# Kernel optimization log

Hardware: AMD Instinct MI355X
Metric: run time of the kernel (lower is better)

## Reference

```python
import jax, jax.numpy as jnp
import numpy as np

NMS_THR = 0.3


def pairwise_iou(b):
    # b: [N,4] in x1,y1,x2,y2
    area = (b[:, 2] - b[:, 0]) * (b[:, 3] - b[:, 1])  # [N]
    x1 = jnp.maximum(b[:, None, 0], b[None, :, 0])
    y1 = jnp.maximum(b[:, None, 1], b[None, :, 1])
    x2 = jnp.minimum(b[:, None, 2], b[None, :, 2])
    y2 = jnp.minimum(b[:, None, 3], b[None, :, 3])
    inter = jnp.clip(x2 - x1, 0.0) * jnp.clip(y2 - y1, 0.0)
    return inter / (area[:, None] + area[None, :] - inter + 1e-9)


def nms_keep(boxes, scores, valid, thr):
    # greedy NMS, fixed-shape: returns bool keep mask in original order
    N = boxes.shape[0]
    order = jnp.argsort(-jnp.where(valid, scores, -jnp.inf))
    b = boxes[order]
    v = valid[order]
    iou = pairwise_iou(b)  # [N,N]

    def step(keep, i):
        suppressed = jnp.any(keep & (iou[i] > thr))
        keep = keep.at[i].set(v[i] & jnp.logical_not(suppressed))
        return keep, None

    keep_sorted, _ = jax.lax.scan(step, jnp.zeros((N,), dtype=bool), jnp.arange(N))
    return jnp.zeros((N,), dtype=bool).at[order].set(keep_sorted)


def setup_inputs() -> dict:
    key = jax.random.key(0)
    k1, k2, k3, k4 = jax.random.split(key, 4)
    N, C, S = 6000, 81, 800
    # well-formed proposals: x1,y1 in [0, 600), w,h in [8, 200)
    xy = jax.random.uniform(k1, (N, 2), dtype=jnp.float32) * 600.0
    wh = 8.0 + jax.random.uniform(k2, (N, 2), dtype=jnp.float32) * 192.0
    proposals = jnp.concatenate([xy, xy + wh], axis=1)  # [N,4]
    reg = jax.random.normal(k3, (N, C * 4), dtype=jnp.float32)
    clss = jax.random.normal(k4, (N, C), dtype=jnp.float32) * 2.0
    stds = jnp.array([0.1, 0.1, 0.2, 0.2], dtype=jnp.float32)
    return {"proposals": proposals, "reg": reg, "clss": clss, "stds": stds, "img_size": S}


def reference(proposals, reg, clss, stds, img_size):
    N, C = clss.shape
    # anchors_bbox2offset: x1y1x2y2 -> center x,y + w,h
    w = proposals[:, 2] - proposals[:, 0]
    h = proposals[:, 3] - proposals[:, 1]
    cx = proposals[:, 0] + 0.5 * w
    cy = proposals[:, 1] + 0.5 * h
    # class selection
    probs = jax.nn.softmax(clss, axis=1)
    cls_idx = jnp.argmax(probs, axis=1)  # [N]
    score = jnp.take_along_axis(probs, cls_idx[:, None], axis=1)[:, 0]
    valid = cls_idx != 0  # non-background
    reg4 = reg.reshape(N, C, 4)
    t = jnp.take_along_axis(reg4, cls_idx[:, None, None], axis=1)[:, 0, :] * stds  # [N,4]
    # decode
    px = cx + w * t[:, 0]
    py = cy + h * t[:, 1]
    pw = w * jnp.exp(t[:, 2])
    ph = h * jnp.exp(t[:, 3])
    # offset2bbox + clip
    hi = jnp.float32(img_size - 1)
    x1 = jnp.clip(px - 0.5 * pw, 0.0, hi)
    y1 = jnp.clip(py - 0.5 * ph, 0.0, hi)
    x2 = jnp.clip(px + 0.5 * pw, 0.0, hi)
    y2 = jnp.clip(py + 0.5 * ph, 0.0, hi)
    boxes = jnp.stack((x1, y1, x2, y2), axis=1)  # [N,4]
    keep = nms_keep(jax.lax.stop_gradient(boxes), jax.lax.stop_gradient(score), valid, NMS_THR)
    m = keep.astype(boxes.dtype)
    return boxes * m[:, None], score * m, cls_idx * keep.astype(cls_idx.dtype)
```

## Files before the change

### kernel.cpp

```cpp
#include <hip/hip_runtime.h>
#include <math.h>

#define NMS_THR 0.3f
#define NACC 8

__device__ __forceinline__ float fmul(float a, float b){ return __fmul_rn(a,b); }
__device__ __forceinline__ float fadd(float a, float b){ return __fadd_rn(a,b); }
__device__ __forceinline__ float fsub(float a, float b){ return __fsub_rn(a,b); }

#define BAR_LDS() asm volatile("s_waitcnt lgkmcnt(0)\n\ts_barrier" ::: "memory")

__device__ __forceinline__ unsigned long long rfl64(unsigned long long x){
    unsigned int lo = (unsigned int)__builtin_amdgcn_readfirstlane((int)(unsigned int)x);
    unsigned int hi = (unsigned int)__builtin_amdgcn_readfirstlane((int)(unsigned int)(x >> 32));
    return ((unsigned long long)hi << 32) | lo;
}

__global__ __launch_bounds__(256) void k_decode(
    const float* __restrict__ prop, const float* __restrict__ reg,
    const float* __restrict__ clss, const float* __restrict__ stds,
    const int* __restrict__ imgsz,
    float* __restrict__ boxes, float* __restrict__ key,
    float* __restrict__ score, int* __restrict__ cls,
    int N, int C)
{
    int wid  = threadIdx.x >> 6;
    int lane = threadIdx.x & 63;
    int n = blockIdx.x * 4 + wid;
    if (n >= N) return;
    const float* row = clss + (long)n * C;
    float ninf = -__builtin_inff();
    float x0 = (lane < C)      ? row[lane]      : ninf;
    float x1 = (lane + 64 < C) ? row[lane + 64] : ninf;
    float m = fmaxf(x0, x1);
    for (int o = 32; o > 0; o >>= 1) m = fmaxf(m, __shfl_xor(m, o));
    float e0 = (lane < C)      ? expf(x0 - m) : 0.0f;
    float e1 = (lane + 64 < C) ? expf(x1 - m) : 0.0f;
    float s = e0 + e1;
    for (int o = 32; o > 0; o >>= 1) s += __shfl_xor(s, o);
    float bv; int bi;
    if (e0 >= e1) { bv = e0; bi = lane; } else { bv = e1; bi = lane + 64; }
    for (int o = 32; o > 0; o >>= 1) {
        float ov = __shfl_xor(bv, o);
        int   oi = __shfl_xor(bi, o);
        if (ov > bv || (ov == bv && oi < bi)) { bv = ov; bi = oi; }
    }
    if (lane == 0) {
        float sc = 1.0f / s;
        int   c  = bi;
        int   valid = (c != 0);
        float p0 = prop[n*4+0], p1 = prop[n*4+1], p2 = prop[n*4+2], p3 = prop[n*4+3];
        float w  = fsub(p2, p0), h = fsub(p3, p1);
        float cx = fadd(p0, fmul(0.5f, w));
        float cy = fadd(p1, fmul(0.5f, h));
        const float* rr = reg + (long)n * C * 4 + (long)c * 4;
        float t0 = fmul(rr[0], stds[0]);
        float t1 = fmul(rr[1], stds[1]);
        float t2 = fmul(rr[2], stds[2]);
        float t3 = fmul(rr[3], stds[3]);
        float px = fadd(cx, fmul(w, t0));
        float py = fadd(cy, fmul(h, t1));
        float pw = fmul(w, expf(t2));
        float ph = fmul(h, expf(t3));
        float hi = (float)(imgsz[0] - 1);
        float bx1 = fminf(fmaxf(fsub(px, fmul(0.5f, pw)), 0.0f), hi);
        float by1 = fminf(fmaxf(fsub(py, fmul(0.5f, ph)), 0.0f), hi);
        float bx2 = fminf(fmaxf(fadd(px, fmul(0.5f, pw)), 0.0f), hi);
        float by2 = fminf(fmaxf(fadd(py, fmul(0.5f, ph)), 0.0f), hi);
        boxes[n*4+0]=bx1; boxes[n*4+1]=by1; boxes[n*4+2]=bx2; boxes[n*4+3]=by2;
        score[n] = sc;
        cls[n]   = c;
        key[n]   = valid ? sc : ninf;
    }
}

__global__ __launch_bounds__(256) void k_rank(
    const float* __restrict__ key, const float* __restrict__ boxes,
    float* __restrict__ boxesSorted, float* __restrict__ areaSorted,
    float* __restrict__ keySorted, int* __restrict__ rank,
    int* __restrict__ nValidPtr, int N)
{
    extern __shared__ float lkey[];
    __shared__ int part[256];
    int tid = threadIdx.x;
    for (int j = tid; j < N; j += 256) lkey[j] = key[j];
    __syncthreads();

    int i = blockIdx.x * 64 + (tid & 63);
    int s = tid >> 6;
    int Q = (N + 3) >> 2;
    int r_part = 0;
    if (i < N) {
        float ki = lkey[i];
        int j0 = s * Q, j1 = min(N, j0 + Q);
        for (int j = j0; j < j1; ++j) {
            float kj = lkey[j];
            r_part += (kj > ki) || (kj == ki && j < i);
        }
    }
    part[tid] = r_part;
    __syncthreads();

    if (tid < 64 && i < N) {
        int r = part[tid] + part[tid+64] + part[tid+128] + part[tid+192];
        float ki = lkey[i];
        rank[i] = r;
        float b0 = boxes[i*4+0], b1 = boxes[i*4+1], b2 = boxes[i*4+2], b3 = boxes[i*4+3];
        boxesSorted[r*4+0]=b0; boxesSorted[r*4+1]=b1; boxesSorted[r*4+2]=b2; boxesSorted[r*4+3]=b3;
        areaSorted[r] = fmul(fsub(b2,b0), fsub(b3,b1));
        keySorted[r]  = ki;
    }

    if (blockIdx.x == 0) {
        __syncthreads();
        float ninf = -__builtin_inff();
        int inv = 0;
        for (int j = tid; j < N; j += 256) inv += (lkey[j] == ninf);
        part[tid] = inv;
        __syncthreads();
        if (tid == 0) {
            int t = 0;
            for (int q = 0; q < 256; ++q) t += part[q];
            nValidPtr[0] = N - t;
        }
    }
}

__global__ __launch_bounds__(256) void k_mask(
    const float* __restrict__ bs, const float* __restrict__ areas,
    const float* __restrict__ keySorted, unsigned long long* __restrict__ mask,
    unsigned long long* __restrict__ bq,
    int N, int W, int Wpad)
{
    int wid  = threadIdx.x >> 6;
    int lane = threadIdx.x & 63;
    int i = blockIdx.x * 4 + wid;
    if (i >= N) return;
    if (keySorted[i] == -__builtin_inff()) return;
    float ax1 = bs[i*4+0], ay1 = bs[i*4+1], ax2 = bs[i*4+2], ay2 = bs[i*4+3];
    float aa  = areas[i];
    int w0 = i >> 6;
#pragma unroll
    for (int k = 1; k <= 3; ++k) {
        unsigned long long bm = 0ULL;
        if (w0 - k >= 0) {
            int j = (w0 - k) * 64 + lane;
            float bx1 = bs[j*4+0], by1 = bs[j*4+1], bx2 = bs[j*4+2], by2 = bs[j*4+3];
            float ba  = areas[j];
            float ix1 = fmaxf(ax1,bx1), iy1 = fmaxf(ay1,by1);
            float ix2 = fminf(ax2,bx2), iy2 = fminf(ay2,by2);
            float iw = fmaxf(fsub(ix2,ix1), 0.0f);
            float ih = fmaxf(fsub(iy2,iy1), 0.0f);
            float inter = fmul(iw, ih);
            float denom = fadd(fsub(fadd(aa, ba), inter), 1e-9f);
            float iou = inter / denom;
            bm = __ballot(iou > NMS_THR);
        }
        if (lane == 0) bq[(size_t)i*4 + k] = bm;
    }
    for (int w = w0; w < W; ++w) {
        int j = w*64 + lane;
        int bit = 0;
        if (j < N && j != i) {
            float bx1 = bs[j*4+0], by1 = bs[j*4+1], bx2 = bs[j*4+2], by2 = bs[j*4+3];
            float ba  = areas[j];
            float ix1 = fmaxf(ax1,bx1), iy1 = fmaxf(ay1,by1);
            float ix2 = fminf(ax2,bx2), iy2 = fminf(ay2,by2);
            float iw = fmaxf(fsub(ix2,ix1), 0.0f);
            float ih = fmaxf(fsub(iy2,iy1), 0.0f);
            float inter = fmul(iw, ih);
            float denom = fadd(fsub(fadd(aa, ba), inter), 1e-9f);
            float iou = inter / denom;
            bit = (iou > NMS_THR) ? 1 : 0;
        }
        unsigned long long fwd = __ballot(bit && (j > i));
        if (w == w0) {
            unsigned long long bwd = __ballot(bit && (j < i));
            if (lane == 0) {
                mask[(long)i*Wpad + w] = fwd;
                bq[(size_t)i*4 + 0] = bwd;
            }
        } else {
            if (lane == 0) mask[(long)i*Wpad + w] = fwd;
        }
    }
}

__global__ __launch_bounds__((NACC+1)*64, 1) void k_scan(
    const unsigned long long* __restrict__ mask,
    const unsigned long long* __restrict__ bq,
    const int* __restrict__ nValidPtr,
    int* __restrict__ keepSorted, int N, int W, int Wpad)
{
    __shared__ unsigned long long ldsPartA[NACC+1];
    __shared__ unsigned long long ldsPartB[NACC+1];
    __shared__ unsigned long long ldsKeepLo, ldsKeepHi;
    int tid  = threadIdx.x;
    int wid  = tid >> 6;
    int lane = tid & 63;
    for (int i = tid; i < N; i += (NACC+1)*64) keepSorted[i] = 0;
    if (tid <= NACC) { ldsPartA[tid] = 0ULL; ldsPartB[tid] = 0ULL; }
    if (tid == 0) { ldsKeepLo = 0ULL; ldsKeepHi = 0ULL; }
    __syncthreads();

    int nValid  = __builtin_amdgcn_readfirstlane(nValidPtr[0]);
    int nChunks = (nValid + 127) >> 7;

    unsigned long long a0=0,a1=0,a2=0,a3=0, b0=0,b1=0,b2=0,b3=0;
    unsigned long long keepLoPrev = 0ULL, keepHiPrev = 0ULL;
    if (wid == 0 && nChunks > 0) {
        int rA = lane, rB = 64 + lane;
        if (rA < N) {
            ulonglong2 q01 = *(const ulonglong2*)(bq + (size_t)rA*4);
            ulonglong2 q23 = *(const ulonglong2*)(bq + (size_t)rA*4 + 2);
            a0=q01.x; a1=q01.y; a2=q23.x; a3=q23.y;
        }
        if (rB < N) {
            ulonglong2 q01 = *(const ulonglong2*)(bq + (size_t)rB*4);
            ulonglong2 q23 = *(const ulonglong2*)(bq + (size_t)rB*4 + 2);
            b0=q01.x; b1=q01.y; b2=q23.x; b3=q23.y;
        }
    }
    unsigned long long accx = 0ULL, accy = 0ULL;
    bool accWave = (wid >= 1);
    int  accIdx  = wid - 1;
    bool laneok  = (2*lane + 1 < Wpad);

    for (int c = 0; c < nChunks; ++c) {
        int base = c << 7;
        if (wid == 0) {
            unsigned long long na0=0,na1=0,na2=0,na3=0, nb0=0,nb1=0,nb2=0,nb3=0;
            if (c + 1 < nChunks) {
                int rA = base + 128 + lane, rB = base + 192 + lane;
                if (rA < N) {
                    ulonglong2 q01 = *(const ulonglong2*)(bq + (size_t)rA*4);
                    ulonglong2 q23 = *(const ulonglong2*)(bq + (size_t)rA*4 + 2);
                    na0=q01.x; na1=q01.y; na2=q23.x; na3=q23.y;
                }
                if (rB < N) {
                    ulonglong2 q01 = *(const ulonglong2*)(bq + (size_t)rB*4);
                    ulonglong2 q23 = *(const ulonglong2*)(bq + (size_t)rB*4 + 2);
                    nb0=q01.x; nb1=q01.y; nb2=q23.x; nb3=q23.y;
                }
            }

            unsigned long long pA = 0ULL, pB = 0ULL;
#pragma unroll
            for (int k = 1; k <= NACC; ++k) { pA |= ldsPartA[k]; pB |= ldsPartB[k]; }
            unsigned long long prevLo =
                __ballot(((a1 & keepHiPrev) | (a2 & keepLoPrev)) != 0ULL);
            unsigned long long prevHi =
                __ballot(((b2 & keepHiPrev) | (b3 & keepLoPrev)) != 0ULL);
            unsigned long long incLo = rfl64(pA) | prevLo;
            unsigned long long incHi = rfl64(pB) | prevHi;
            int nv  = nValid - base;
            unsigned long long validLo = (nv >= 64) ? ~0ULL : ((1ULL << nv) - 1ULL);
            int nv2 = nv - 64;
            unsigned long long validHi = (nv2 >= 64) ? ~0ULL
                                        : (nv2 <= 0 ? 0ULL : ((1ULL << nv2) - 1ULL));
            unsigned long long candLo = validLo & ~incLo;
            unsigned long long candHi = validHi & ~incHi;
            unsigned long long keepLo = 0ULL, keepHi = 0ULL;

            while (candLo) {
                int f = __builtin_ctzll(candLo);
                unsigned long long sup = __ballot(((a0 >> f) & 1ULL) != 0ULL);
                unsigned long long b = 1ULL << f;
                keepLo |= b;
                candLo &= ~sup & ~b;
            }
            candHi &= ~__ballot((b1 & keepLo) != 0ULL);
            while (candHi) {
                int f = __builtin_ctzll(candHi);
                unsigned long long sup = __ballot(((b0 >> f) & 1ULL) != 0ULL);
                unsigned long long b = 1ULL << f;
                keepHi |= b;
                candHi &= ~sup & ~b;
            }
            keepLoPrev = keepLo; keepHiPrev = keepHi;
            if (lane == 0) { ldsKeepLo = keepLo; ldsKeepHi = keepHi; }
            if (base + lane < N)      keepSorted[base + lane]      = (int)((keepLo >> lane) & 1ULL);
            if (base + 64 + lane < N) keepSorted[base + 64 + lane] = (int)((keepHi >> lane) & 1ULL);
            a0=na0; a1=na1; a2=na2; a3=na3; b0=nb0; b1=nb1; b2=nb2; b3=nb3;
        }
        BAR_LDS();
        unsigned long long kLo = ldsKeepLo;
        unsigned long long kHi = ldsKeepHi;
        if (accWave && laneok && lane == c + 1) {
            ldsPartA[wid] = accx;
            ldsPartB[wid] = accy;
        }
        BAR_LDS();
        if (accWave && laneok) {
            unsigned int myb = (accIdx < 4)
                ? (unsigned int)((kLo >> (16*accIdx)) & 0xFFFFULL)
                : (unsigned int)((kHi >> (16*(accIdx-4))) & 0xFFFFULL);
            if (myb) {
                const unsigned long long* mb =
                    mask + (size_t)(base + 16*accIdx) * Wpad + 2*lane;
                unsigned int b = myb;
                int q0 = __builtin_ctz(b); b &= b - 1;
                int q1=-1,q2=-1,q3=-1,q4=-1,q5=-1,q6=-1,q7=-1;
                if (b) { q1 = __builtin_ctz(b); b &= b - 1; }
                if (b) { q2 = __builtin_ctz(b); b &= b - 1; }
                if (b) { q3 = __builtin_ctz(b); b &= b - 1; }
                if (b) { q4 = __builtin_ctz(b); b &= b - 1; }
                if (b) { q5 = __builtin_ctz(b); b &= b - 1; }
                if (b) { q6 = __builtin_ctz(b); b &= b - 1; }
                if (b) { q7 = __builtin_ctz(b); b &= b - 1; }
                ulonglong2 v0 = {0,0}, v1 = {0,0}, v2 = {0,0}, v3 = {0,0};
                ulonglong2 v4 = {0,0}, v5 = {0,0}, v6 = {0,0}, v7 = {0,0};
                v0 = *(const ulonglong2*)(mb + (size_t)q0 * Wpad);
                if (q1 >= 0) v1 = *(const ulonglong2*)(mb + (size_t)q1 * Wpad);
                if (q2 >= 0) v2 = *(const ulonglong2*)(mb + (size_t)q2 * Wpad);
                if (q3 >= 0) v3 = *(const ulonglong2*)(mb + (size_t)q3 * Wpad);
                if (q4 >= 0) v4 = *(const ulonglong2*)(mb + (size_t)q4 * Wpad);
                if (q5 >= 0) v5 = *(const ulonglong2*)(mb + (size_t)q5 * Wpad);
                if (q6 >= 0) v6 = *(const ulonglong2*)(mb + (size_t)q6 * Wpad);
                if (q7 >= 0) v7 = *(const ulonglong2*)(mb + (size_t)q7 * Wpad);
                accx |= ((v0.x|v1.x)|(v2.x|v3.x)) | ((v4.x|v5.x)|(v6.x|v7.x));
                accy |= ((v0.y|v1.y)|(v2.y|v3.y)) | ((v4.y|v5.y)|(v6.y|v7.y));
                while (b) {
                    int a = __builtin_ctz(b); b &= b - 1;
                    ulonglong2 v = *(const ulonglong2*)(mb + (size_t)a * Wpad);
                    accx |= v.x; accy |= v.y;
                }
            }
        }
    }
}

__global__ __launch_bounds__(256) void k_out(
    const float* __restrict__ boxes, const float* __restrict__ score,
    const int* __restrict__ cls, const int* __restrict__ rank,
    const int* __restrict__ keepSorted,
    float* __restrict__ out, int N)
{
    int n = blockIdx.x * blockDim.x + threadIdx.x;
    if (n >= N) return;
    int k = keepSorted[rank[n]];
    float m = (float)k;
    out[n*4+0] = boxes[n*4+0]*m;
    out[n*4+1] = boxes[n*4+1]*m;
    out[n*4+2] = boxes[n*4+2]*m;
    out[n*4+3] = boxes[n*4+3]*m;
    out[(long)N*4 + n] = score[n]*m;
    out[(long)N*5 + n] = (float)(cls[n] * k);
}

extern "C" void kernel_launch(void* const* d_in, const int* in_sizes, int n_in,
                              void* d_out, int out_size, void* d_ws, size_t ws_size,
                              hipStream_t stream) {
    const float* prop = (const float*)d_in[0];
    const float* reg  = (const float*)d_in[1];
    const float* clss = (const float*)d_in[2];
    const float* stds = (const float*)d_in[3];
    const int*   img  = (const int*)d_in[4];

    int N = in_sizes[0] / 4;
    int C = in_sizes[2] / N;
    int W = (N + 63) / 64;
    int Wpad = (W + 1) & ~1;

    char* ws = (char*)d_ws;
    size_t off = 0;
    float* boxes       = (float*)(ws + off); off += (size_t)N*4*sizeof(float);
    float* key         = (float*)(ws + off); off += (size_t)N*sizeof(float);
    float* score       = (float*)(ws + off); off += (size_t)N*sizeof(float);
    int*   cls         = (int*)  (ws + off); off += (size_t)N*sizeof(int);
    int*   rank        = (int*)  (ws + off); off += (size_t)N*sizeof(int);
    float* boxesSorted = (float*)(ws + off); off += (size_t)N*4*sizeof(float);
    float* areaSorted  = (float*)(ws + off); off += (size_t)N*sizeof(float);
    float* keySorted   = (float*)(ws + off); off += (size_t)N*sizeof(float);
    int*   keepSorted  = (int*)  (ws + off); off += (size_t)N*sizeof(int);
    int*   nValid      = (int*)  (ws + off); off += sizeof(int);
    off = (off + 31) & ~(size_t)31;
    unsigned long long* bq    = (unsigned long long*)(ws + off);
    off += (size_t)N * 4 * sizeof(unsigned long long);
    unsigned long long* mask  = (unsigned long long*)(ws + off);
    off += (size_t)N * Wpad * sizeof(unsigned long long);
    (void)ws_size; (void)out_size; (void)n_in;

    int rowBlocks  = (N + 3) / 4;
    int thrBlocks  = (N + 255) / 256;
    int rankBlocks = (N + 63) / 64;

    k_decode<<<rowBlocks, 256, 0, stream>>>(prop, reg, clss, stds, img,
                                            boxes, key, score, cls, N, C);
    k_rank<<<rankBlocks, 256, (size_t)N*sizeof(float), stream>>>(key, boxes,
                                            boxesSorted, areaSorted, keySorted, rank, nValid, N);
    k_mask<<<rowBlocks, 256, 0, stream>>>(boxesSorted, areaSorted, keySorted,
                                          mask, bq, N, W, Wpad);
    k_scan<<<1, (NACC+1)*64, 0, stream>>>(mask, bq, nValid, keepSorted, N, W, Wpad);
    k_out<<<thrBlocks, 256, 0, stream>>>(boxes, score, cls, rank, keepSorted,
                                         (float*)d_out, N);
}
```

Measured before the change: 170.7 us.

## Fuse five NMS kernels into one cooperative persistent kernel with grid syncs

```diff
diff --git a/kernel.cpp b/kernel.cpp
--- a/kernel.cpp
+++ b/kernel.cpp
@@ -1,8 +1,13 @@
 #include <hip/hip_runtime.h>
+#include <hip/hip_cooperative_groups.h>
 #include <math.h>
+
+namespace cg = cooperative_groups;
 
 #define NMS_THR 0.3f
 #define NACC 8
+#define NBLK 256
+#define NTHR 576
 
 __device__ __forceinline__ float fmul(float a, float b){ return __fmul_rn(a,b); }
 __device__ __forceinline__ float fadd(float a, float b){ return __fadd_rn(a,b); }
@@ -16,347 +21,338 @@
     return ((unsigned long long)hi << 32) | lo;
 }
 
-__global__ __launch_bounds__(256) void k_decode(
-    const float* __restrict__ prop, const float* __restrict__ reg,
-    const float* __restrict__ clss, const float* __restrict__ stds,
-    const int* __restrict__ imgsz,
-    float* __restrict__ boxes, float* __restrict__ key,
-    float* __restrict__ score, int* __restrict__ cls,
-    int N, int C)
+struct Params {
+    const float *prop, *reg, *clss, *stds;
+    const int *img;
+    float *boxes, *key, *score;
+    int *cls, *rank;
+    float *boxesSorted, *areaSorted, *keySorted;
+    int *keepSorted, *nValid;
+    unsigned long long *bq, *mask;
+    float *out;
+    int N, C, W, Wpad, rankBlocks;
+};
+
+__global__ __launch_bounds__(NTHR, 1) void k_all(Params p)
 {
-    int wid  = threadIdx.x >> 6;
-    int lane = threadIdx.x & 63;
-    int n = blockIdx.x * 4 + wid;
-    if (n >= N) return;
-    const float* row = clss + (long)n * C;
-    float ninf = -__builtin_inff();
-    float x0 = (lane < C)      ? row[lane]      : ninf;
-    float x1 = (lane + 64 < C) ? row[lane + 64] : ninf;
-    float m = fmaxf(x0, x1);
-    for (int o = 32; o > 0; o >>= 1) m = fmaxf(m, __shfl_xor(m, o));
-    float e0 = (lane < C)      ? expf(x0 - m) : 0.0f;
-    float e1 = (lane + 64 < C) ? expf(x1 - m) : 0.0f;
-    float s = e0 + e1;
-    for (int o = 32; o > 0; o >>= 1) s += __shfl_xor(s, o);
-    float bv; int bi;
-    if (e0 >= e1) { bv = e0; bi = lane; } else { bv = e1; bi = lane + 64; }
-    for (int o = 32; o > 0; o >>= 1) {
-        float ov = __shfl_xor(bv, o);
-        int   oi = __shfl_xor(bi, o);
-        if (ov > bv || (ov == bv && oi < bi)) { bv = ov; bi = oi; }
-    }
-    if (lane == 0) {
-        float sc = 1.0f / s;
-        int   c  = bi;
-        int   valid = (c != 0);
-        float p0 = prop[n*4+0], p1 = prop[n*4+1], p2 = prop[n*4+2], p3 = prop[n*4+3];
-        float w  = fsub(p2, p0), h = fsub(p3, p1);
-        float cx = fadd(p0, fmul(0.5f, w));
-        float cy = fadd(p1, fmul(0.5f, h));
-        const float* rr = reg + (long)n * C * 4 + (long)c * 4;
-        float t0 = fmul(rr[0], stds[0]);
-        float t1 = fmul(rr[1], stds[1]);
-        float t2 = fmul(rr[2], stds[2]);
-        float t3 = fmul(rr[3], stds[3]);
-        float px = fadd(cx, fmul(w, t0));
-        float py = fadd(cy, fmul(h, t1));
-        float pw = fmul(w, expf(t2));
-        float ph = fmul(h, expf(t3));
-        float hi = (float)(imgsz[0] - 1);
-        float bx1 = fminf(fmaxf(fsub(px, fmul(0.5f, pw)), 0.0f), hi);
-        float by1 = fminf(fmaxf(fsub(py, fmul(0.5f, ph)), 0.0f), hi);
-        float bx2 = fminf(fmaxf(fadd(px, fmul(0.5f, pw)), 0.0f), hi);
-        float by2 = fminf(fmaxf(fadd(py, fmul(0.5f, ph)), 0.0f), hi);
-        boxes[n*4+0]=bx1; boxes[n*4+1]=by1; boxes[n*4+2]=bx2; boxes[n*4+3]=by2;
-        score[n] = sc;
-        cls[n]   = c;
-        key[n]   = valid ? sc : ninf;
-    }
-}
-
-__global__ __launch_bounds__(256) void k_rank(
-    const float* __restrict__ key, const float* __restrict__ boxes,
-    float* __restrict__ boxesSorted, float* __restrict__ areaSorted,
-    float* __restrict__ keySorted, int* __restrict__ rank,
-    int* __restrict__ nValidPtr, int N)
-{
-    extern __shared__ float lkey[];
-    __shared__ int part[256];
-    int tid = threadIdx.x;
-    for (int j = tid; j < N; j += 256) lkey[j] = key[j];
-    __syncthreads();
-
-    int i = blockIdx.x * 64 + (tid & 63);
-    int s = tid >> 6;
-    int Q = (N + 3) >> 2;
-    int r_part = 0;
-    if (i < N) {
-        float ki = lkey[i];
-        int j0 = s * Q, j1 = min(N, j0 + Q);
-        for (int j = j0; j < j1; ++j) {
-            float kj = lkey[j];
-            r_part += (kj > ki) || (kj == ki && j < i);
-        }
-    }
-    part[tid] = r_part;
-    __syncthreads();
-
-    if (tid < 64 && i < N) {
-        int r = part[tid] + part[tid+64] + part[tid+128] + part[tid+192];
-        float ki = lkey[i];
-        rank[i] = r;
-        float b0 = boxes[i*4+0], b1 = boxes[i*4+1], b2 = boxes[i*4+2], b3 = boxes[i*4+3];
-        boxesSorted[r*4+0]=b0; boxesSorted[r*4+1]=b1; boxesSorted[r*4+2]=b2; boxesSorted[r*4+3]=b3;
-        areaSorted[r] = fmul(fsub(b2,b0), fsub(b3,b1));
-        keySorted[r]  = ki;
-    }
-
-    if (blockIdx.x == 0) {
+    cg::grid_group grid = cg::this_grid();
+    extern __shared__ char smem[];
+    const int tid  = threadIdx.x;
+    const int bid  = blockIdx.x;
+    const int wi   = tid >> 6;
+    const int lane = tid & 63;
+    const int gwave  = bid * (NTHR/64) + wi;
+    const int nWaves = gridDim.x * (NTHR/64);
+    const int N = p.N, C = p.C, W = p.W, Wpad = p.Wpad;
+    const float ninf = -__builtin_inff();
+
+    for (int n = gwave; n < N; n += nWaves) {
+        const float* row = p.clss + (long)n * C;
+        float x0 = (lane < C)      ? row[lane]      : ninf;
+        float x1 = (lane + 64 < C) ? row[lane + 64] : ninf;
+        float m = fmaxf(x0, x1);
+        for (int o = 32; o > 0; o >>= 1) m = fmaxf(m, __shfl_xor(m, o));
+        float e0 = (lane < C)      ? expf(x0 - m) : 0.0f;
+        float e1 = (lane + 64 < C) ? expf(x1 - m) : 0.0f;
+        float s = e0 + e1;
+        for (int o = 32; o > 0; o >>= 1) s += __shfl_xor(s, o);
+        float bv; int bi;
+        if (e0 >= e1) { bv = e0; bi = lane; } else { bv = e1; bi = lane + 64; }
+        for (int o = 32; o > 0; o >>= 1) {
+            float ov = __shfl_xor(bv, o);
+            int   oi = __shfl_xor(bi, o);
+            if (ov > bv || (ov == bv && oi < bi)) { bv = ov; bi = oi; }
+        }
+        if (lane == 0) {
+            float sc = 1.0f / s;
+            int   c  = bi;
+            int   valid = (c != 0);
+            float p0 = p.prop[n*4+0], p1 = p.prop[n*4+1];
+            float p2 = p.prop[n*4+2], p3 = p.prop[n*4+3];
+            float w  = fsub(p2, p0), h = fsub(p3, p1);
+            float cx = fadd(p0, fmul(0.5f, w));
+            float cy = fadd(p1, fmul(0.5f, h));
+            const float* rr = p.reg + (long)n * C * 4 + (long)c * 4;
+            float t0 = fmul(rr[0], p.stds[0]);
+            float t1 = fmul(rr[1], p.stds[1]);
+            float t2 = fmul(rr[2], p.stds[2]);
+            float t3 = fmul(rr[3], p.stds[3]);
+            float px = fadd(cx, fmul(w, t0));
+            float py = fadd(cy, fmul(h, t1));
+            float pw = fmul(w, expf(t2));
+            float ph = fmul(h, expf(t3));
+            float hi = (float)(p.img[0] - 1);
+            float bx1 = fminf(fmaxf(fsub(px, fmul(0.5f, pw)), 0.0f), hi);
+            float by1 = fminf(fmaxf(fsub(py, fmul(0.5f, ph)), 0.0f), hi);
+            float bx2 = fminf(fmaxf(fadd(px, fmul(0.5f, pw)), 0.0f), hi);
+            float by2 = fminf(fmaxf(fadd(py, fmul(0.5f, ph)), 0.0f), hi);
+            p.boxes[n*4+0]=bx1; p.boxes[n*4+1]=by1;
+            p.boxes[n*4+2]=bx2; p.boxes[n*4+3]=by2;
+            p.score[n] = sc;
+            p.cls[n]   = c;
+            p.key[n]   = valid ? sc : ninf;
+        }
+    }
+    grid.sync();
+
+    {
+        float* lkey = (float*)smem;
+        int*   part = (int*)(smem + (size_t)N*sizeof(float));
+        if (bid < p.rankBlocks) {
+            for (int j = tid; j < N; j += NTHR) lkey[j] = p.key[j];
+            __syncthreads();
+            int i = bid * 64 + lane;
+            int Q = (N + 8) / 9;
+            int r_part = 0;
+            if (i < N) {
+                float ki = lkey[i];
+                int j0 = wi * Q, j1 = min(N, j0 + Q);
+                for (int j = j0; j < j1; ++j) {
+                    float kj = lkey[j];
+                    r_part += (kj > ki) || (kj == ki && j < i);
+                }
+            }
+            part[tid] = r_part;
+            __syncthreads();
+            if (tid < 64 && i < N) {
+                int r = 0;
+#pragma unroll
+                for (int sIdx = 0; sIdx < 9; ++sIdx) r += part[tid + 64*sIdx];
+                float ki = lkey[i];
+                p.rank[i] = r;
+                float b0 = p.boxes[i*4+0], b1 = p.boxes[i*4+1];
+                float b2 = p.boxes[i*4+2], b3 = p.boxes[i*4+3];
+                p.boxesSorted[r*4+0]=b0; p.boxesSorted[r*4+1]=b1;
+                p.boxesSorted[r*4+2]=b2; p.boxesSorted[r*4+3]=b3;
+                p.areaSorted[r] = fmul(fsub(b2,b0), fsub(b3,b1));
+                p.keySorted[r]  = ki;
+            }
+            if (bid == 0) {
+                __syncthreads();
+                int inv = 0;
+                for (int j = tid; j < N; j += NTHR) inv += (lkey[j] == ninf);
+                part[tid] = inv;
+                __syncthreads();
+                if (tid == 0) {
+                    int t = 0;
+                    for (int q = 0; q < NTHR; ++q) t += part[q];
+                    p.nValid[0] = N - t;
+                }
+            }
+        }
+    }
+    grid.sync();
+
+    for (int i = gwave; i < N; i += nWaves) {
+        if (p.keySorted[i] == ninf) continue;
+        const float* bs = p.boxesSorted;
+        float ax1 = bs[i*4+0], ay1 = bs[i*4+1], ax2 = bs[i*4+2], ay2 = bs[i*4+3];
+        float aa  = p.areaSorted[i];
+        int w0 = i >> 6;
+#pragma unroll
+        for (int k = 1; k <= 3; ++k) {
+            unsigned long long bm = 0ULL;
+            if (w0 - k >= 0) {
+                int j = (w0 - k) * 64 + lane;
+                float bx1 = bs[j*4+0], by1 = bs[j*4+1], bx2 = bs[j*4+2], by2 = bs[j*4+3];
+                float ba  = p.areaSorted[j];
+                float ix1 = fmaxf(ax1,bx1), iy1 = fmaxf(ay1,by1);
+                float ix2 = fminf(ax2,bx2), iy2 = fminf(ay2,by2);
+                float iw = fmaxf(fsub(ix2,ix1), 0.0f);
+                float ih = fmaxf(fsub(iy2,iy1), 0.0f);
+                float inter = fmul(iw, ih);
+                float denom = fadd(fsub(fadd(aa, ba), inter), 1e-9f);
+                float iou = inter / denom;
+                bm = __ballot(iou > NMS_THR);
+            }
+            if (lane == 0) p.bq[(size_t)i*4 + k] = bm;
+        }
+        for (int w = w0; w < W; ++w) {
+            int j = w*64 + lane;
+            int bit = 0;
+            if (j < N && j != i) {
+                float bx1 = bs[j*4+0], by1 = bs[j*4+1], bx2 = bs[j*4+2], by2 = bs[j*4+3];
+                float ba  = p.areaSorted[j];
+                float ix1 = fmaxf(ax1,bx1), iy1 = fmaxf(ay1,by1);
+                float ix2 = fminf(ax2,bx2), iy2 = fminf(ay2,by2);
+                float iw = fmaxf(fsub(ix2,ix1), 0.0f);
+                float ih = fmaxf(fsub(iy2,iy1), 0.0f);
+                float inter = fmul(iw, ih);
+                float denom = fadd(fsub(fadd(aa, ba), inter), 1e-9f);
+                float iou = inter / denom;
+                bit = (iou > NMS_THR) ? 1 : 0;
+            }
+            unsigned long long fwd = __ballot(bit && (j > i));
+            if (w == w0) {
+                unsigned long long bwd = __ballot(bit && (j < i));
+                if (lane == 0) {
+                    p.mask[(long)i*Wpad + w] = fwd;
+                    p.bq[(size_t)i*4 + 0] = bwd;
+                }
+            } else {
+                if (lane == 0) p.mask[(long)i*Wpad + w] = fwd;
+            }
+        }
+    }
+    grid.sync();
+
+    if (bid == 0) {
+        __shared__ unsigned long long ldsPartA[NACC+1];
+        __shared__ unsigned long long ldsPartB[NACC+1];
+        __shared__ unsigned long long ldsKeepLo, ldsKeepHi;
+        const unsigned long long* mask = p.mask;
+        const unsigned long long* bq   = p.bq;
+        int* keepSorted = p.keepSorted;
+        for (int i = tid; i < N; i += NTHR) keepSorted[i] = 0;
+        if (tid <= NACC) { ldsPartA[tid] = 0ULL; ldsPartB[tid] = 0ULL; }
+        if (tid == 0) { ldsKeepLo = 0ULL; ldsKeepHi = 0ULL; }
         __syncthreads();
-        float ninf = -__builtin_inff();
-        int inv = 0;
-        for (int j = tid; j < N; j += 256) inv += (lkey[j] == ninf);
-        part[tid] = inv;
-        __syncthreads();
-        if (tid == 0) {
-            int t = 0;
-            for (int q = 0; q < 256; ++q) t += part[q];
-            nValidPtr[0] = N - t;
-        }
-    }
-}
-
-__global__ __launch_bounds__(256) void k_mask(
-    const float* __restrict__ bs, const float* __restrict__ areas,
-    const float* __restrict__ keySorted, unsigned long long* __restrict__ mask,
-    unsigned long long* __restrict__ bq,
-    int N, int W, int Wpad)
-{
-    int wid  = threadIdx.x >> 6;
-    int lane = threadIdx.x & 63;
-    int i = blockIdx.x * 4 + wid;
-    if (i >= N) return;
-    if (keySorted[i] == -__builtin_inff()) return;
-    float ax1 = bs[i*4+0], ay1 = bs[i*4+1], ax2 = bs[i*4+2], ay2 = bs[i*4+3];
-    float aa  = areas[i];
-    int w0 = i >> 6;
+
+        int nValid  = __builtin_amdgcn_readfirstlane(p.nValid[0]);
+        int nChunks = (nValid + 127) >> 7;
+
+        unsigned long long a0=0,a1=0,a2=0,a3=0, b0=0,b1=0,b2=0,b3=0;
+        unsigned long long keepLoPrev = 0ULL, keepHiPrev = 0ULL;
+        if (wi == 0 && nChunks > 0) {
+            int rA = lane, rB = 64 + lane;
+            if (rA < N) {
+                ulonglong2 q01 = *(const ulonglong2*)(bq + (size_t)rA*4);
+                ulonglong2 q23 = *(const ulonglong2*)(bq + (size_t)rA*4 + 2);
+                a0=q01.x; a1=q01.y; a2=q23.x; a3=q23.y;
+            }
+            if (rB < N) {
+                ulonglong2 q01 = *(const ulonglong2*)(bq + (size_t)rB*4);
+                ulonglong2 q23 = *(const ulonglong2*)(bq + (size_t)rB*4 + 2);
+                b0=q01.x; b1=q01.y; b2=q23.x; b3=q23.y;
+            }
+        }
+        unsigned long long accx = 0ULL, accy = 0ULL;
+        bool accWave = (wi >= 1);
+        int  accIdx  = wi - 1;
+        bool laneok  = (2*lane + 1 < Wpad);
+
+        for (int c = 0; c < nChunks; ++c) {
+            int base = c << 7;
+            if (wi == 0) {
+                unsigned long long na0=0,na1=0,na2=0,na3=0, nb0=0,nb1=0,nb2=0,nb3=0;
+                if (c + 1 < nChunks) {
+                    int rA = base + 128 + lane, rB = base + 192 + lane;
+                    if (rA < N) {
+                        ulonglong2 q01 = *(const ulonglong2*)(bq + (size_t)rA*4);
+                        ulonglong2 q23 = *(const ulonglong2*)(bq + (size_t)rA*4 + 2);
+                        na0=q01.x; na1=q01.y; na2=q23.x; na3=q23.y;
+                    }
+                    if (rB < N) {
+                        ulonglong2 q01 = *(const ulonglong2*)(bq + (size_t)rB*4);
+                        ulonglong2 q23 = *(const ulonglong2*)(bq + (size_t)rB*4 + 2);
+                        nb0=q01.x; nb1=q01.y; nb2=q23.x; nb3=q23.y;
+                    }
+                }
+
+                unsigned long long pA = 0ULL, pB = 0ULL;
 #pragma unroll
-    for (int k = 1; k <= 3; ++k) {
-        unsigned long long bm = 0ULL;
-        if (w0 - k >= 0) {
-            int j = (w0 - k) * 64 + lane;
-            float bx1 = bs[j*4+0], by1 = bs[j*4+1], bx2 = bs[j*4+2], by2 = bs[j*4+3];
-            float ba  = areas[j];
-            float ix1 = fmaxf(ax1,bx1), iy1 = fmaxf(ay1,by1);
-            float ix2 = fminf(ax2,bx2), iy2 = fminf(ay2,by2);
-            float iw = fmaxf(fsub(ix2,ix1), 0.0f);
-            float ih = fmaxf(fsub(iy2,iy1), 0.0f);
-            float inter = fmul(iw, ih);
-            float denom = fadd(fsub(fadd(aa, ba), inter), 1e-9f);
-            float iou = inter / denom;
-            bm = __ballot(iou > NMS_THR);
-        }
-        if (lane == 0) bq[(size_t)i*4 + k] = bm;
-    }
-    for (int w = w0; w < W; ++w) {
-        int j = w*64 + lane;
-        int bit = 0;
-        if (j < N && j != i) {
-            float bx1 = bs[j*4+0], by1 = bs[j*4+1], bx2 = bs[j*4+2], by2 = bs[j*4+3];
-            float ba  = areas[j];
-            float ix1 = fmaxf(ax1,bx1), iy1 = fmaxf(ay1,by1);
-            float ix2 = fminf(ax2,bx2), iy2 = fminf(ay2,by2);
-            float iw = fmaxf(fsub(ix2,ix1), 0.0f);
-            float ih = fmaxf(fsub(iy2,iy1), 0.0f);
-            float inter = fmul(iw, ih);
-            float denom = fadd(fsub(fadd(aa, ba), inter), 1e-9f);
-            float iou = inter / denom;
-            bit = (iou > NMS_THR) ? 1 : 0;
-        }
-        unsigned long long fwd = __ballot(bit && (j > i));
-        if (w == w0) {
-            unsigned long long bwd = __ballot(bit && (j < i));
-            if (lane == 0) {
-                mask[(long)i*Wpad + w] = fwd;
-                bq[(size_t)i*4 + 0] = bwd;
-            }
-        } else {
-            if (lane == 0) mask[(long)i*Wpad + w] = fwd;
-        }
-    }
-}
-
-__global__ __launch_bounds__((NACC+1)*64, 1) void k_scan(
-    const unsigned long long* __restrict__ mask,
-    const unsigned long long* __restrict__ bq,
-    const int* __restrict__ nValidPtr,
-    int* __restrict__ keepSorted, int N, int W, int Wpad)
-{
-    __shared__ unsigned long long ldsPartA[NACC+1];
-    __shared__ unsigned long long ldsPartB[NACC+1];
-    __shared__ unsigned long long ldsKeepLo, ldsKeepHi;
-    int tid  = threadIdx.x;
-    int wid  = tid >> 6;
-    int lane = tid & 63;
-    for (int i = tid; i < N; i += (NACC+1)*64) keepSorted[i] = 0;
-    if (tid <= NACC) { ldsPartA[tid] = 0ULL; ldsPartB[tid] = 0ULL; }
-    if (tid == 0) { ldsKeepLo = 0ULL; ldsKeepHi = 0ULL; }
-    __syncthreads();
-
-    int nValid  = __builtin_amdgcn_readfirstlane(nValidPtr[0]);
-    int nChunks = (nValid + 127) >> 7;
-
-    unsigned long long a0=0,a1=0,a2=0,a3=0, b0=0,b1=0,b2=0,b3=0;
-    unsigned long long keepLoPrev = 0ULL, keepHiPrev = 0ULL;
-    if (wid == 0 && nChunks > 0) {
-        int rA = lane, rB = 64 + lane;
-        if (rA < N) {
-            ulonglong2 q01 = *(const ulonglong2*)(bq + (size_t)rA*4);
-            ulonglong2 q23 = *(const ulonglong2*)(bq + (size_t)rA*4 + 2);
-            a0=q01.x; a1=q01.y; a2=q23.x; a3=q23.y;
-        }
-        if (rB < N) {
-            ulonglong2 q01 = *(const ulonglong2*)(bq + (size_t)rB*4);
-            ulonglong2 q23 = *(const ulonglong2*)(bq + (size_t)rB*4 + 2);
-            b0=q01.x; b1=q01.y; b2=q23.x; b3=q23.y;
-        }
-    }
-    unsigned long long accx = 0ULL, accy = 0ULL;
-    bool accWave = (wid >= 1);
-    int  accIdx  = wid - 1;
-    bool laneok  = (2*lane + 1 < Wpad);
-
-    for (int c = 0; c < nChunks; ++c) {
-        int base = c << 7;
-        if (wid == 0) {
-            unsigned long long na0=0,na1=0,na2=0,na3=0, nb0=0,nb1=0,nb2=0,nb3=0;
-            if (c + 1 < nChunks) {
-                int rA = base + 128 + lane, rB = base + 192 + lane;
-                if (rA < N) {
-                    ulonglong2 q01 = *(const ulonglong2*)(bq + (size_t)rA*4);
-                    ulonglong2 q23 = *(const ulonglong2*)(bq + (size_t)rA*4 + 2);
-                    na0=q01.x; na1=q01.y; na2=q23.x; na3=q23.y;
-                }
-                if (rB < N) {
-                    ulonglong2 q01 = *(const ulonglong2*)(bq + (size_t)rB*4);
-                    ulonglong2 q23 = *(const ulonglong2*)(bq + (size_t)rB*4 + 2);
-                    nb0=q01.x; nb1=q01.y; nb2=q23.x; nb3=q23.y;
-                }
-            }
-
-            unsigned long long pA = 0ULL, pB = 0ULL;
-#pragma unroll
-            for (int k = 1; k <= NACC; ++k) { pA |= ldsPartA[k]; pB |= ldsPartB[k]; }
-            unsigned long long prevLo =
-                __ballot(((a1 & keepHiPrev) | (a2 & keepLoPrev)) != 0ULL);
-            unsigned long long prevHi =
-                __ballot(((b2 & keepHiPrev) | (b3 & keepLoPrev)) != 0ULL);
-            unsigned long long incLo = rfl64(pA) | prevLo;
-            unsigned long long incHi = rfl64(pB) | prevHi;
-            int nv  = nValid - base;
-            unsigned long long validLo = (nv >= 64) ? ~0ULL : ((1ULL << nv) - 1ULL);
-            int nv2 = nv - 64;
-            unsigned long long validHi = (nv2 >= 64) ? ~0ULL
-                                        : (nv2 <= 0 ? 0ULL : ((1ULL << nv2) - 1ULL));
-            unsigned long long candLo = validLo & ~incLo;
-            unsigned long long candHi = validHi & ~incHi;
-            unsigned long long keepLo = 0ULL, keepHi = 0ULL;
-
-            while (candLo) {
-                int f = __builtin_ctzll(candLo);
-                unsigned long long sup = __ballot(((a0 >> f) & 1ULL) != 0ULL);
-                unsigned long long b = 1ULL << f;
-                keepLo |= b;
-                candLo &= ~sup & ~b;
-            }
-            candHi &= ~__ballot((b1 & keepLo) != 0ULL);
-            while (candHi) {
-                int f = __builtin_ctzll(candHi);
-                unsigned long long sup = __ballot(((b0 >> f) & 1ULL) != 0ULL);
-                unsigned long long b = 1ULL << f;
-                keepHi |= b;
-                candHi &= ~sup & ~b;
-            }
-            keepLoPrev = keepLo; keepHiPrev = keepHi;
-            if (lane == 0) { ldsKeepLo = keepLo; ldsKeepHi = keepHi; }
-            if (base + lane < N)      keepSorted[base + lane]      = (int)((keepLo >> lane) & 1ULL);
-            if (base + 64 + lane < N) keepSorted[base + 64 + lane] = (int)((keepHi >> lane) & 1ULL);
-            a0=na0; a1=na1; a2=na2; a3=na3; b0=nb0; b1=nb1; b2=nb2; b3=nb3;
-        }
-        BAR_LDS();
-        unsigned long long kLo = ldsKeepLo;
-        unsigned long long kHi = ldsKeepHi;
-        if (accWave && laneok && lane == c + 1) {
-            ldsPartA[wid] = accx;
-            ldsPartB[wid] = accy;
-        }
-        BAR_LDS();
-        if (accWave && laneok) {
-            unsigned int myb = (accIdx < 4)
-                ? (unsigned int)((kLo >> (16*accIdx)) & 0xFFFFULL)
-                : (unsigned int)((kHi >> (16*(accIdx-4))) & 0xFFFFULL);
-            if (myb) {
-                const unsigned long long* mb =
-                    mask + (size_t)(base + 16*accIdx) * Wpad + 2*lane;
-                unsigned int b = myb;
-                int q0 = __builtin_ctz(b); b &= b - 1;
-                int q1=-1,q2=-1,q3=-1,q4=-1,q5=-1,q6=-1,q7=-1;
-                if (b) { q1 = __builtin_ctz(b); b &= b - 1; }
-                if (b) { q2 = __builtin_ctz(b); b &= b - 1; }
-                if (b) { q3 = __builtin_ctz(b); b &= b - 1; }
-                if (b) { q4 = __builtin_ctz(b); b &= b - 1; }
-                if (b) { q5 = __builtin_ctz(b); b &= b - 1; }
-                if (b) { q6 = __builtin_ctz(b); b &= b - 1; }
-                if (b) { q7 = __builtin_ctz(b); b &= b - 1; }
-                ulonglong2 v0 = {0,0}, v1 = {0,0}, v2 = {0,0}, v3 = {0,0};
-                ulonglong2 v4 = {0,0}, v5 = {0,0}, v6 = {0,0}, v7 = {0,0};
-                v0 = *(const ulonglong2*)(mb + (size_t)q0 * Wpad);
-                if (q1 >= 0) v1 = *(const ulonglong2*)(mb + (size_t)q1 * Wpad);
-                if (q2 >= 0) v2 = *(const ulonglong2*)(mb + (size_t)q2 * Wpad);
-                if (q3 >= 0) v3 = *(const ulonglong2*)(mb + (size_t)q3 * Wpad);
-                if (q4 >= 0) v4 = *(const ulonglong2*)(mb + (size_t)q4 * Wpad);
-                if (q5 >= 0) v5 = *(const ulonglong2*)(mb + (size_t)q5 * Wpad);
-                if (q6 >= 0) v6 = *(const ulonglong2*)(mb + (size_t)q6 * Wpad);
-                if (q7 >= 0) v7 = *(const ulonglong2*)(mb + (size_t)q7 * Wpad);
-                accx |= ((v0.x|v1.x)|(v2.x|v3.x)) | ((v4.x|v5.x)|(v6.x|v7.x));
-                accy |= ((v0.y|v1.y)|(v2.y|v3.y)) | ((v4.y|v5.y)|(v6.y|v7.y));
-                while (b) {
-                    int a = __builtin_ctz(b); b &= b - 1;
-                    ulonglong2 v = *(const ulonglong2*)(mb + (size_t)a * Wpad);
-                    accx |= v.x; accy |= v.y;
-                }
-            }
-        }
-    }
-}
-
-__global__ __launch_bounds__(256) void k_out(
-    const float* __restrict__ boxes, const float* __restrict__ score,
-    const int* __restrict__ cls, const int* __restrict__ rank,
-    const int* __restrict__ keepSorted,
-    float* __restrict__ out, int N)
-{
-    int n = blockIdx.x * blockDim.x + threadIdx.x;
-    if (n >= N) return;
-    int k = keepSorted[rank[n]];
-    float m = (float)k;
-    out[n*4+0] = boxes[n*4+0]*m;
-    out[n*4+1] = boxes[n*4+1]*m;
-    out[n*4+2] = boxes[n*4+2]*m;
-    out[n*4+3] = boxes[n*4+3]*m;
-    out[(long)N*4 + n] = score[n]*m;
-    out[(long)N*5 + n] = (float)(cls[n] * k);
+                for (int k = 1; k <= NACC; ++k) { pA |= ldsPartA[k]; pB |= ldsPartB[k]; }
+                unsigned long long prevLo =
+                    __ballot(((a1 & keepHiPrev) | (a2 & keepLoPrev)) != 0ULL);
+                unsigned long long prevHi =
+                    __ballot(((b2 & keepHiPrev) | (b3 & keepLoPrev)) != 0ULL);
+                unsigned long long incLo = rfl64(pA) | prevLo;
+                unsigned long long incHi = rfl64(pB) | prevHi;
+                int nv  = nValid - base;
+                unsigned long long validLo = (nv >= 64) ? ~0ULL : ((1ULL << nv) - 1ULL);
+                int nv2 = nv - 64;
+                unsigned long long validHi = (nv2 >= 64) ? ~0ULL
+                                            : (nv2 <= 0 ? 0ULL : ((1ULL << nv2) - 1ULL));
+                unsigned long long candLo = validLo & ~incLo;
+                unsigned long long candHi = validHi & ~incHi;
+                unsigned long long keepLo = 0ULL, keepHi = 0ULL;
+
+                while (candLo) {
+                    int f = __builtin_ctzll(candLo);
+                    unsigned long long sup = __ballot(((a0 >> f) & 1ULL) != 0ULL);
+                    unsigned long long b = 1ULL << f;
+                    keepLo |= b;
+                    candLo &= ~sup & ~b;
+                }
+                candHi &= ~__ballot((b1 & keepLo) != 0ULL);
+                while (candHi) {
+                    int f = __builtin_ctzll(candHi);
+                    unsigned long long sup = __ballot(((b0 >> f) & 1ULL) != 0ULL);
+                    unsigned long long b = 1ULL << f;
+                    keepHi |= b;
+                    candHi &= ~sup & ~b;
+                }
+                keepLoPrev = keepLo; keepHiPrev = keepHi;
+                if (lane == 0) { ldsKeepLo = keepLo; ldsKeepHi = keepHi; }
+                if (base + lane < N)
+                    keepSorted[base + lane]      = (int)((keepLo >> lane) & 1ULL);
+                if (base + 64 + lane < N)
+                    keepSorted[base + 64 + lane] = (int)((keepHi >> lane) & 1ULL);
+                a0=na0; a1=na1; a2=na2; a3=na3; b0=nb0; b1=nb1; b2=nb2; b3=nb3;
+            }
+            BAR_LDS();
+            unsigned long long kLo = ldsKeepLo;
+            unsigned long long kHi = ldsKeepHi;
+            if (accWave && laneok && lane == c + 1) {
+                ldsPartA[wi] = accx;
+                ldsPartB[wi] = accy;
+            }
+            BAR_LDS();
+            if (accWave && laneok) {
+                unsigned int myb = (accIdx < 4)
+                    ? (unsigned int)((kLo >> (16*accIdx)) & 0xFFFFULL)
+                    : (unsigned int)((kHi >> (16*(accIdx-4))) & 0xFFFFULL);
+                if (myb) {
+                    const unsigned long long* mb =
+                        mask + (size_t)(base + 16*accIdx) * Wpad + 2*lane;
+                    unsigned int b = myb;
+                    int q0 = __builtin_ctz(b); b &= b - 1;
+                    int q1=-1,q2=-1,q3=-1,q4=-1,q5=-1,q6=-1,q7=-1;
+                    if (b) { q1 = __builtin_ctz(b); b &= b - 1; }
+                    if (b) { q2 = __builtin_ctz(b); b &= b - 1; }
+                    if (b) { q3 = __builtin_ctz(b); b &= b - 1; }
+                    if (b) { q4 = __builtin_ctz(b); b &= b - 1; }
+                    if (b) { q5 = __builtin_ctz(b); b &= b - 1; }
+                    if (b) { q6 = __builtin_ctz(b); b &= b - 1; }
+                    if (b) { q7 = __builtin_ctz(b); b &= b - 1; }
+                    ulonglong2 v0 = {0,0}, v1 = {0,0}, v2 = {0,0}, v3 = {0,0};
+                    ulonglong2 v4 = {0,0}, v5 = {0,0}, v6 = {0,0}, v7 = {0,0};
+                    v0 = *(const ulonglong2*)(mb + (size_t)q0 * Wpad);
+                    if (q1 >= 0) v1 = *(const ulonglong2*)(mb + (size_t)q1 * Wpad);
+                    if (q2 >= 0) v2 = *(const ulonglong2*)(mb + (size_t)q2 * Wpad);
+                    if (q3 >= 0) v3 = *(const ulonglong2*)(mb + (size_t)q3 * Wpad);
+                    if (q4 >= 0) v4 = *(const ulonglong2*)(mb + (size_t)q4 * Wpad);
+                    if (q5 >= 0) v5 = *(const ulonglong2*)(mb + (size_t)q5 * Wpad);
+                    if (q6 >= 0) v6 = *(const ulonglong2*)(mb + (size_t)q6 * Wpad);
+                    if (q7 >= 0) v7 = *(const ulonglong2*)(mb + (size_t)q7 * Wpad);
+                    accx |= ((v0.x|v1.x)|(v2.x|v3.x)) | ((v4.x|v5.x)|(v6.x|v7.x));
+                    accy |= ((v0.y|v1.y)|(v2.y|v3.y)) | ((v4.y|v5.y)|(v6.y|v7.y));
+                    while (b) {
+                        int a = __builtin_ctz(b); b &= b - 1;
+                        ulonglong2 v = *(const ulonglong2*)(mb + (size_t)a * Wpad);
+                        accx |= v.x; accy |= v.y;
+                    }
+                }
+            }
+        }
+    }
+    grid.sync();
+
+    for (int n = bid * NTHR + tid; n < N; n += gridDim.x * NTHR) {
+        int k = p.keepSorted[p.rank[n]];
+        float m = (float)k;
+        p.out[n*4+0] = p.boxes[n*4+0]*m;
+        p.out[n*4+1] = p.boxes[n*4+1]*m;
+        p.out[n*4+2] = p.boxes[n*4+2]*m;
+        p.out[n*4+3] = p.boxes[n*4+3]*m;
+        p.out[(long)N*4 + n] = p.score[n]*m;
+        p.out[(long)N*5 + n] = (float)(p.cls[n] * k);
+    }
 }
 
 extern "C" void kernel_launch(void* const* d_in, const int* in_sizes, int n_in,
                               void* d_out, int out_size, void* d_ws, size_t ws_size,
                               hipStream_t stream) {
-    const float* prop = (const float*)d_in[0];
-    const float* reg  = (const float*)d_in[1];
-    const float* clss = (const float*)d_in[2];
-    const float* stds = (const float*)d_in[3];
-    const int*   img  = (const int*)d_in[4];
-
     int N = in_sizes[0] / 4;
     int C = in_sizes[2] / N;
     int W = (N + 63) / 64;
@@ -364,34 +360,32 @@
 
     char* ws = (char*)d_ws;
     size_t off = 0;
-    float* boxes       = (float*)(ws + off); off += (size_t)N*4*sizeof(float);
-    float* key         = (float*)(ws + off); off += (size_t)N*sizeof(float);
-    float* score       = (float*)(ws + off); off += (size_t)N*sizeof(float);
-    int*   cls         = (int*)  (ws + off); off += (size_t)N*sizeof(int);
-    int*   rank        = (int*)  (ws + off); off += (size_t)N*sizeof(int);
-    float* boxesSorted = (float*)(ws + off); off += (size_t)N*4*sizeof(float);
-    float* areaSorted  = (float*)(ws + off); off += (size_t)N*sizeof(float);
-    float* keySorted   = (float*)(ws + off); off += (size_t)N*sizeof(float);
-    int*   keepSorted  = (int*)  (ws + off); off += (size_t)N*sizeof(int);
-    int*   nValid      = (int*)  (ws + off); off += sizeof(int);
+    Params p;
+    p.prop = (const float*)d_in[0];
+    p.reg  = (const float*)d_in[1];
+    p.clss = (const float*)d_in[2];
+    p.stds = (const float*)d_in[3];
+    p.img  = (const int*)d_in[4];
+    p.boxes       = (float*)(ws + off); off += (size_t)N*4*sizeof(float);
+    p.key         = (float*)(ws + off); off += (size_t)N*sizeof(float);
+    p.score       = (float*)(ws + off); off += (size_t)N*sizeof(float);
+    p.cls         = (int*)  (ws + off); off += (size_t)N*sizeof(int);
+    p.rank        = (int*)  (ws + off); off += (size_t)N*sizeof(int);
+    p.boxesSorted = (float*)(ws + off); off += (size_t)N*4*sizeof(float);
+    p.areaSorted  = (float*)(ws + off); off += (size_t)N*sizeof(float);
+    p.keySorted   = (float*)(ws + off); off += (size_t)N*sizeof(float);
+    p.keepSorted  = (int*)  (ws + off); off += (size_t)N*sizeof(int);
+    p.nValid      = (int*)  (ws + off); off += sizeof(int);
     off = (off + 31) & ~(size_t)31;
-    unsigned long long* bq    = (unsigned long long*)(ws + off);
-    off += (size_t)N * 4 * sizeof(unsigned long long);
-    unsigned long long* mask  = (unsigned long long*)(ws + off);
-    off += (size_t)N * Wpad * sizeof(unsigned long long);
+    p.bq   = (unsigned long long*)(ws + off); off += (size_t)N * 4 * sizeof(unsigned long long);
+    p.mask = (unsigned long long*)(ws + off); off += (size_t)N * Wpad * sizeof(unsigned long long);
+    p.out  = (float*)d_out;
+    p.N = N; p.C = C; p.W = W; p.Wpad = Wpad;
+    p.rankBlocks = (N + 63) / 64;
     (void)ws_size; (void)out_size; (void)n_in;
 
-    int rowBlocks  = (N + 3) / 4;
-    int thrBlocks  = (N + 255) / 256;
-    int rankBlocks = (N + 63) / 64;
-
-    k_decode<<<rowBlocks, 256, 0, stream>>>(prop, reg, clss, stds, img,
-                                            boxes, key, score, cls, N, C);
-    k_rank<<<rankBlocks, 256, (size_t)N*sizeof(float), stream>>>(key, boxes,
-                                            boxesSorted, areaSorted, keySorted, rank, nValid, N);
-    k_mask<<<rowBlocks, 256, 0, stream>>>(boxesSorted, areaSorted, keySorted,
-                                          mask, bq, N, W, Wpad);
-    k_scan<<<1, (NACC+1)*64, 0, stream>>>(mask, bq, nValid, keepSorted, N, W, Wpad);
-    k_out<<<thrBlocks, 256, 0, stream>>>(boxes, score, cls, rank, keepSorted,
-                                         (float*)d_out, N);
+    size_t smemBytes = (size_t)N * sizeof(float) + NTHR * sizeof(int);
+    void* args[] = { &p };
+    hipLaunchCooperativeKernel((void*)k_all, dim3(NBLK), dim3(NTHR),
+                               args, (unsigned int)smemBytes, stream);
 }
```

Result: slower. 297.8 us (+74.5%).
